# Kernel tuning notes

Measured on AMD Instinct MI355X. Metric: run time of the kernel, lower is better.

## Reference

```python
import jax, jax.numpy as jnp
import numpy as np

N_NODES = 100000
F_DIM = 128      # graph.num_node_features
TE_DIM = 32      # te_emb_dim
D = F_DIM + TE_DIM  # attention embed_dim = 160
B = 4096         # number of target nodes (batched python loop)
K = 64           # candidates per target
TAU = 1.0
THRESHOLD = 0.2
EPS = 1e-10


def setup_inputs() -> dict:
    key = jax.random.key(0)
    ks = jax.random.split(key, 16)
    inp = {
        "x": jax.random.normal(ks[0], (N_NODES, F_DIM), dtype=jnp.float32),
        "target_node_ids": jax.random.randint(ks[1], (B,), 0, N_NODES),
        "target_node_times": jax.random.randint(ks[2], (B,), 1, 10000),
        "neighbor_ids": jax.random.randint(ks[3], (B, K), 0, N_NODES),
        "edge_time": jax.random.randint(ks[4], (B, K), 0, 10000),
        "edge_weight": jax.random.uniform(ks[5], (B, K), dtype=jnp.float32),
        "gumbel_u": jax.random.uniform(ks[6], (B, K), dtype=jnp.float32),
        # TemporalEncoding params: te(t) = cos(t * w + b)
        "te_w": jax.random.normal(ks[7], (TE_DIM,), dtype=jnp.float32),
        "te_b": jax.random.normal(ks[8], (TE_DIM,), dtype=jnp.float32),
        # MultiheadAttention params (packed qkv like torch)
        "in_proj_w": jax.random.normal(ks[9], (3 * D, D), dtype=jnp.float32) / np.sqrt(D),
        "in_proj_b": jnp.zeros((3 * D,), dtype=jnp.float32),
        "out_w": jax.random.normal(ks[10], (D, D), dtype=jnp.float32) / np.sqrt(D),
        "out_b": jnp.zeros((D,), dtype=jnp.float32),
        # MLP: Linear(D+1 -> 1) + LeakyReLU
        "mlp_w": jax.random.normal(ks[11], (D + 1,), dtype=jnp.float32) / np.sqrt(D + 1),
        "mlp_b": jnp.zeros((1,), dtype=jnp.float32),
    }
    return inp


def reference(x, target_node_ids, target_node_times, neighbor_ids, edge_time,
              edge_weight, gumbel_u, te_w, te_b, in_proj_w, in_proj_b,
              out_w, out_b, mlp_w, mlp_b):
    # --- build target embedding: [B, D]
    t_x = x[target_node_ids]                                          # [B, F]
    t_te = jnp.cos(target_node_times[:, None].astype(jnp.float32) * te_w + te_b)  # [B, TE]
    q_in = jnp.concatenate([t_x, t_te], axis=-1)                      # [B, D]

    # --- candidate embeddings: [B, K, D]
    c_x = x[neighbor_ids]                                             # [B, K, F]
    c_te = jnp.cos(edge_time[..., None].astype(jnp.float32) * te_w + te_b)        # [B, K, TE]
    kv_in = jnp.concatenate([c_x, c_te], axis=-1)                     # [B, K, D]

    # --- single-head MultiheadAttention (eval mode, 1 query per target)
    Wq, Wk, Wv = in_proj_w[:D], in_proj_w[D:2 * D], in_proj_w[2 * D:]
    bq, bk, bv = in_proj_b[:D], in_proj_b[D:2 * D], in_proj_b[2 * D:]
    q = q_in @ Wq.T + bq                                              # [B, D]
    k = jnp.einsum('bkf,df->bkd', kv_in, Wk) + bk                     # [B, K, D]
    v = jnp.einsum('bkf,df->bkd', kv_in, Wv) + bv                     # [B, K, D]
    scores = jnp.einsum('bd,bkd->bk', q, k) / jnp.sqrt(jnp.float32(D))
    attn_w = jax.nn.softmax(scores, axis=-1)                          # [B, K]
    ctx = jnp.einsum('bk,bkd->bd', attn_w, v)                         # [B, D]
    attn_output = ctx @ out_w.T + out_b                               # [B, D]

    # --- gumbel-softmax mask over attention weights (soft, then threshold)
    g = -jnp.log(-jnp.log(gumbel_u + EPS) + EPS)                      # gumbel(0,1)
    y_soft = jax.nn.softmax((attn_w + g) / TAU, axis=-1)
    candidate_mask = y_soft > THRESHOLD                               # [B, K] bool

    # --- MLP edge-weight update: Linear(D+1 -> 1) + LeakyReLU
    mlp_in = jnp.concatenate(
        [jnp.broadcast_to(attn_output[:, None, :], (attn_output.shape[0], edge_weight.shape[1], attn_output.shape[1])),
         edge_weight[..., None]], axis=-1)                            # [B, K, D+1]
    new_edge_weight = jax.nn.leaky_relu(jnp.einsum('bkf,f->bk', mlp_in, mlp_w) + mlp_b[0])  # [B, K]

    return attn_output, new_edge_weight, candidate_mask
```

## Files before the change

kernel.cpp:

```cpp
#include <hip/hip_runtime.h>

#define F_DIM 128
#define TE_DIM 32
#define DD 160
#define NB 4096
#define KK 64
#define ROWS 4
#define LD 164
#define TE_STRIDE 36

#define WS_M   0
#define WS_V2  25600
#define WS_C   51200
#define WS_U   51360
#define WS_B2  51520
#define WS_S0  51680
#define WS_TOT 51681

__device__ __forceinline__ float dot4acc(const float4 w, const float4 v, float a) {
    a = fmaf(w.x, v.x, a);
    a = fmaf(w.y, v.y, a);
    a = fmaf(w.z, v.z, a);
    a = fmaf(w.w, v.w, a);
    return a;
}

__device__ __forceinline__ float wave_max(float v) {
    #pragma unroll
    for (int off = 32; off > 0; off >>= 1) v = fmaxf(v, __shfl_xor(v, off, 64));
    return v;
}
__device__ __forceinline__ float wave_sum(float v) {
    #pragma unroll
    for (int off = 32; off > 0; off >>= 1) v += __shfl_xor(v, off, 64);
    return v;
}

__device__ __forceinline__ void gemv_rows(
    const float* __restrict__ W, const float* __restrict__ bias,
    const float (*vin)[LD], float (*vout)[LD], int tid)
{
    const int r  = tid & 3;
    const int dl = tid >> 2;
    const float4* v4 = (const float4*)vin[r];
    const float4* w0 = (const float4*)(W + (long)dl * DD);
    const float4* w1 = (const float4*)(W + (long)(dl + 64) * DD);
    float a0 = bias[dl];
    float a1 = bias[dl + 64];
    if (dl < 32) {
        const float4* w2 = (const float4*)(W + (long)(dl + 128) * DD);
        float a2 = bias[dl + 128];
        #pragma unroll 8
        for (int f = 0; f < 40; ++f) {
            const float4 v = v4[f];
            a0 = dot4acc(w0[f], v, a0);
            a1 = dot4acc(w1[f], v, a1);
            a2 = dot4acc(w2[f], v, a2);
        }
        vout[r][dl]       = a0;
        vout[r][dl + 64]  = a1;
        vout[r][dl + 128] = a2;
    } else {
        #pragma unroll 8
        for (int f = 0; f < 40; ++f) {
            const float4 v = v4[f];
            a0 = dot4acc(w0[f], v, a0);
            a1 = dot4acc(w1[f], v, a1);
        }
        vout[r][dl]      = a0;
        vout[r][dl + 64] = a1;
    }
}

__global__ __launch_bounds__(256)
void setup_kernel(const float* __restrict__ ipw, const float* __restrict__ ipb,
                  const float* __restrict__ ow,  const float* __restrict__ ob,
                  float* __restrict__ ws)
{
    const int blk = blockIdx.x;
    const int t   = threadIdx.x;
    const float inv = 0.07905694150420949f;

    __shared__ float s_vec[DD];

    if (blk < DD) {
        const float* wk = ipw + DD * DD;
        if (t < DD) s_vec[t] = wk[(long)t * DD + blk];
        __syncthreads();
        if (t < DD) {
            float a0 = 0.f, a1 = 0.f, a2 = 0.f, a3 = 0.f;
            #pragma unroll 4
            for (int d = 0; d < DD; d += 4) {
                a0 = fmaf(s_vec[d],     ipw[(long)d * DD + t],       a0);
                a1 = fmaf(s_vec[d + 1], ipw[(long)(d + 1) * DD + t], a1);
                a2 = fmaf(s_vec[d + 2], ipw[(long)(d + 2) * DD + t], a2);
                a3 = fmaf(s_vec[d + 3], ipw[(long)(d + 3) * DD + t], a3);
            }
            ws[WS_M + blk * DD + t] = (a0 + a1 + a2 + a3) * inv;
        }
    } else if (blk < 2 * DD) {
        const int i = blk - DD;
        const float* wv = ipw + 2 * DD * DD;
        if (t < DD) s_vec[t] = ow[(long)i * DD + t];
        __syncthreads();
        if (t < DD) {
            float a0 = 0.f, a1 = 0.f, a2 = 0.f, a3 = 0.f;
            #pragma unroll 4
            for (int d = 0; d < DD; d += 4) {
                a0 = fmaf(s_vec[d],     wv[(long)d * DD + t],       a0);
                a1 = fmaf(s_vec[d + 1], wv[(long)(d + 1) * DD + t], a1);
                a2 = fmaf(s_vec[d + 2], wv[(long)(d + 2) * DD + t], a2);
                a3 = fmaf(s_vec[d + 3], wv[(long)(d + 3) * DD + t], a3);
            }
            ws[WS_V2 + i * DD + t] = a0 + a1 + a2 + a3;
        }
    } else if (blk == 2 * DD) {
        const float* wk = ipw + DD * DD;
        if (t < DD) s_vec[t] = ipb[t];
        __syncthreads();
        if (t < DD) {
            float a0 = 0.f, a1 = 0.f, a2 = 0.f, a3 = 0.f;
            #pragma unroll 4
            for (int d = 0; d < DD; d += 4) {
                a0 = fmaf(s_vec[d],     wk[(long)d * DD + t],       a0);
                a1 = fmaf(s_vec[d + 1], wk[(long)(d + 1) * DD + t], a1);
                a2 = fmaf(s_vec[d + 2], wk[(long)(d + 2) * DD + t], a2);
                a3 = fmaf(s_vec[d + 3], wk[(long)(d + 3) * DD + t], a3);
            }
            ws[WS_C + t] = (a0 + a1 + a2 + a3) * inv;
        }
    } else if (blk == 2 * DD + 1) {
        if (t < DD) s_vec[t] = ipb[DD + t];
        __syncthreads();
        if (t < DD) {
            float a0 = 0.f, a1 = 0.f, a2 = 0.f, a3 = 0.f;
            #pragma unroll 4
            for (int d = 0; d < DD; d += 4) {
                a0 = fmaf(s_vec[d],     ipw[(long)d * DD + t],       a0);
                a1 = fmaf(s_vec[d + 1], ipw[(long)(d + 1) * DD + t], a1);
                a2 = fmaf(s_vec[d + 2], ipw[(long)(d + 2) * DD + t], a2);
                a3 = fmaf(s_vec[d + 3], ipw[(long)(d + 3) * DD + t], a3);
            }
            ws[WS_U + t] = (a0 + a1 + a2 + a3) * inv;
        }
    } else {
        if (t < DD) s_vec[t] = ipb[2 * DD + t];
        __syncthreads();
        if (t < DD) {
            const float* owr = ow + (long)t * DD;
            float a0 = 0.f, a1 = 0.f, a2 = 0.f, a3 = 0.f;
            #pragma unroll 4
            for (int d = 0; d < DD; d += 4) {
                a0 = fmaf(s_vec[d],     owr[d],     a0);
                a1 = fmaf(s_vec[d + 1], owr[d + 1], a1);
                a2 = fmaf(s_vec[d + 2], owr[d + 2], a2);
                a3 = fmaf(s_vec[d + 3], owr[d + 3], a3);
            }
            ws[WS_B2 + t] = ob[t] + (a0 + a1 + a2 + a3);
        }
        if (t >= 192) {
            const int lane = t - 192;
            float p = ipb[lane] * ipb[DD + lane];
            p = fmaf(ipb[lane + 64], ipb[DD + lane + 64], p);
            if (lane < 32) p = fmaf(ipb[lane + 128], ipb[DD + lane + 128], p);
            const float s = wave_sum(p);
            if (lane == 0) ws[WS_S0] = s * inv;
        }
    }
}

__global__ __launch_bounds__(256, 4)
void structure_learner_kernel(
    const float* __restrict__ x,
    const int*   __restrict__ target_node_ids,
    const int*   __restrict__ target_node_times,
    const int*   __restrict__ neighbor_ids,
    const int*   __restrict__ edge_time,
    const float* __restrict__ edge_weight,
    const float* __restrict__ gumbel_u,
    const float* __restrict__ te_w,
    const float* __restrict__ te_b,
    const float* __restrict__ mlp_w,
    const float* __restrict__ mlp_b,
    const float* __restrict__ ws,
    float* __restrict__ out_ao,
    float* __restrict__ out_new,
    float* __restrict__ out_mask)
{
    __shared__ __attribute__((aligned(16))) float s_qin[ROWS][LD];
    __shared__ __attribute__((aligned(16))) float s_qt[ROWS][LD];
    __shared__ __attribute__((aligned(16))) float s_wkv[ROWS][LD];
    __shared__ __attribute__((aligned(16))) float s_ao[ROWS][LD];
    __shared__ float s_attnw[ROWS][KK];
    __shared__ int   s_nid[ROWS][KK];
    __shared__ __attribute__((aligned(4))) _Float16 s_te[ROWS][KK][TE_STRIDE];

    const int tid  = threadIdx.x;
    const int wr   = tid >> 6;
    const int lane = tid & 63;
    const int b    = blockIdx.x * ROWS + wr;

    const float* Mw = ws + WS_M;
    const float* V2 = ws + WS_V2;
    const float* Cv = ws + WS_C;
    const float* Uv = ws + WS_U;
    const float* B2 = ws + WS_B2;
    const float  s0 = ws[WS_S0];

    {
        s_nid[wr][lane] = neighbor_ids[(long)b * KK + lane];
        const float etv = (float)edge_time[(long)b * KK + lane];
        const int tn = target_node_ids[b];
        const float2 tx = *(const float2*)(x + (long)tn * F_DIM + lane * 2);
        s_qin[wr][lane * 2]     = tx.x;
        s_qin[wr][lane * 2 + 1] = tx.y;
        if (lane < TE_DIM) {
            const float tt = (float)target_node_times[b];
            s_qin[wr][F_DIM + lane] = cosf(tt * te_w[lane] + te_b[lane]);
        }
        #pragma unroll
        for (int jj = 0; jj < 16; ++jj) {
            union { _Float16 h[2]; unsigned u; } pk;
            pk.h[0] = (_Float16)cosf(etv * te_w[2 * jj]     + te_b[2 * jj]);
            pk.h[1] = (_Float16)cosf(etv * te_w[2 * jj + 1] + te_b[2 * jj + 1]);
            *(unsigned*)&s_te[wr][lane][2 * jj] = pk.u;
        }
    }
    __syncthreads();

    gemv_rows(Mw, Cv, s_qin, s_qt, tid);
    __syncthreads();

    float aw;
    {
        float p = s_qin[wr][lane] * Uv[lane];
        p = fmaf(s_qin[wr][lane + 64], Uv[lane + 64], p);
        if (lane < 32) p = fmaf(s_qin[wr][128 + lane], Uv[128 + lane], p);
        const float sbk = wave_sum(p) + s0;

        const int nidk = s_nid[wr][lane];
        const float4* xr  = (const float4*)(x + (long)nidk * F_DIM);
        const float4* qt4 = (const float4*)s_qt[wr];
        float acc = 0.f;
        #pragma unroll 8
        for (int f = 0; f < F_DIM / 4; ++f)
            acc = dot4acc(xr[f], qt4[f], acc);
        const float* qte = s_qt[wr] + F_DIM;
        #pragma unroll
        for (int jj = 0; jj < 16; ++jj) {
            union { _Float16 h[2]; unsigned u; } pk;
            pk.u = *(const unsigned*)&s_te[wr][lane][2 * jj];
            acc = fmaf(qte[2 * jj],     (float)pk.h[0], acc);
            acc = fmaf(qte[2 * jj + 1], (float)pk.h[1], acc);
        }
        const float sc = acc + sbk;
        const float m = wave_max(sc);
        const float e = expf(sc - m);
        const float l = wave_sum(e);
        aw = e / l;
        s_attnw[wr][lane] = aw;
    }

    {
        float ax = 0.f, ay = 0.f, at = 0.f;
        const float* xb = x + lane * 2;
        const int lte = lane & 31;
        #pragma unroll 8
        for (int k = 0; k < KK; ++k) {
            const float wgt = s_attnw[wr][k];
            const int   nid = s_nid[wr][k];
            const float2 xv = *(const float2*)(xb + (long)nid * F_DIM);
            ax = fmaf(wgt, xv.x, ax);
            ay = fmaf(wgt, xv.y, ay);
            at = fmaf(wgt, (float)s_te[wr][k][lte], at);
        }
        s_wkv[wr][lane * 2]     = ax;
        s_wkv[wr][lane * 2 + 1] = ay;
        if (lane < TE_DIM) s_wkv[wr][F_DIM + lane] = at;
    }
    __syncthreads();

    gemv_rows(V2, B2, s_wkv, s_ao, tid);
    __syncthreads();

    {
        float p = s_ao[wr][lane] * mlp_w[lane];
        p = fmaf(s_ao[wr][lane + 64], mlp_w[lane + 64], p);
        if (lane < 32) p = fmaf(s_ao[wr][lane + 128], mlp_w[lane + 128], p);
        const float base = wave_sum(p) + mlp_b[0];

        float* ao = out_ao + (long)b * DD;
        ao[lane]      = s_ao[wr][lane];
        ao[lane + 64] = s_ao[wr][lane + 64];
        if (lane < 32) ao[lane + 128] = s_ao[wr][lane + 128];

        const float u = gumbel_u[(long)b * KK + lane];
        const float g = -logf(-logf(u + 1e-10f) + 1e-10f);
        const float z = aw + g;
        const float m = wave_max(z);
        const float e = expf(z - m);
        const float l = wave_sum(e);
        out_mask[(long)b * KK + lane] = (e / l > 0.2f) ? 1.0f : 0.0f;

        const float ew  = edge_weight[(long)b * KK + lane];
        const float val = fmaf(ew, mlp_w[DD], base);
        out_new[(long)b * KK + lane] = (val >= 0.f) ? val : 0.01f * val;
    }
}

extern "C" void kernel_launch(void* const* d_in, const int* in_sizes, int n_in,
                              void* d_out, int out_size, void* d_ws, size_t ws_size,
                              hipStream_t stream) {
    const float* x   = (const float*)d_in[0];
    const int*   tni = (const int*)d_in[1];
    const int*   tnt = (const int*)d_in[2];
    const int*   nid = (const int*)d_in[3];
    const int*   et  = (const int*)d_in[4];
    const float* ew  = (const float*)d_in[5];
    const float* gu  = (const float*)d_in[6];
    const float* tew = (const float*)d_in[7];
    const float* teb = (const float*)d_in[8];
    const float* ipw = (const float*)d_in[9];
    const float* ipb = (const float*)d_in[10];
    const float* ow  = (const float*)d_in[11];
    const float* ob  = (const float*)d_in[12];
    const float* mw  = (const float*)d_in[13];
    const float* mb  = (const float*)d_in[14];

    float* wsf = (float*)d_ws;

    float* out      = (float*)d_out;
    float* out_ao   = out;
    float* out_new  = out + (long)NB * DD;
    float* out_mask = out + (long)NB * DD + (long)NB * KK;

    setup_kernel<<<2 * DD + 3, 256, 0, stream>>>(ipw, ipb, ow, ob, wsf);

    structure_learner_kernel<<<NB / ROWS, 256, 0, stream>>>(
        x, tni, tnt, nid, et, ew, gu, tew, teb, mw, mb, wsf,
        out_ao, out_new, out_mask);
}
```

Before: 172.6 us.

## Precompute temporal-encoding cosine table in setup kernel and look it up per edge

Adds a 10000x32 cosine lookup table, built by extra setup blocks, so the main kernel reads temporal encodings from the table instead of computing 32 cosf calls per edge. Falls back to direct cosf when the workspace is too small or the time is out of range. Also splits the score dot product into two accumulators and raises the unroll on the weighted-sum loop. Trades transcendental compute for about 1.28 MB of table writes and gathered reads, and the table only covers the integer time range 0 to 9999.

```diff
diff --git a/kernel.cpp b/kernel.cpp
--- a/kernel.cpp
+++ b/kernel.cpp
@@ -15,7 +15,11 @@
 #define WS_U   51360
 #define WS_B2  51520
 #define WS_S0  51680
-#define WS_TOT 51681
+#define WS_TE  51684
+#define TAB_T  10000
+#define TAB_N  (TAB_T * TE_DIM)
+#define TAB_BLOCKS 250
+#define SETUP_BASE (2 * DD + 3)
 
 __device__ __forceinline__ float dot4acc(const float4 w, const float4 v, float a) {
     a = fmaf(w.x, v.x, a);
@@ -75,6 +79,7 @@
 __global__ __launch_bounds__(256)
 void setup_kernel(const float* __restrict__ ipw, const float* __restrict__ ipb,
                   const float* __restrict__ ow,  const float* __restrict__ ob,
+                  const float* __restrict__ te_w, const float* __restrict__ te_b,
                   float* __restrict__ ws)
 {
     const int blk = blockIdx.x;
@@ -82,6 +87,17 @@
     const float inv = 0.07905694150420949f;
 
     __shared__ float s_vec[DD];
+
+    if (blk >= SETUP_BASE) {
+        const int g0 = (blk - SETUP_BASE) * 256 + t;
+        #pragma unroll
+        for (int it = 0; it < 5; ++it) {
+            const int g = g0 + it * (TAB_BLOCKS * 256);
+            const int tt = g >> 5, d = g & 31;
+            ws[WS_TE + g] = cosf(fmaf((float)tt, te_w[d], te_b[d]));
+        }
+        return;
+    }
 
     if (blk < DD) {
         const float* wk = ipw + DD * DD;
@@ -183,6 +199,7 @@
     const float* __restrict__ mlp_w,
     const float* __restrict__ mlp_b,
     const float* __restrict__ ws,
+    const float* __restrict__ tetab,
     float* __restrict__ out_ao,
     float* __restrict__ out_new,
     float* __restrict__ out_mask)
@@ -209,21 +226,38 @@
 
     {
         s_nid[wr][lane] = neighbor_ids[(long)b * KK + lane];
-        const float etv = (float)edge_time[(long)b * KK + lane];
+        const int etv_i = edge_time[(long)b * KK + lane];
         const int tn = target_node_ids[b];
         const float2 tx = *(const float2*)(x + (long)tn * F_DIM + lane * 2);
         s_qin[wr][lane * 2]     = tx.x;
         s_qin[wr][lane * 2 + 1] = tx.y;
         if (lane < TE_DIM) {
-            const float tt = (float)target_node_times[b];
-            s_qin[wr][F_DIM + lane] = cosf(tt * te_w[lane] + te_b[lane]);
-        }
-        #pragma unroll
-        for (int jj = 0; jj < 16; ++jj) {
-            union { _Float16 h[2]; unsigned u; } pk;
-            pk.h[0] = (_Float16)cosf(etv * te_w[2 * jj]     + te_b[2 * jj]);
-            pk.h[1] = (_Float16)cosf(etv * te_w[2 * jj + 1] + te_b[2 * jj + 1]);
-            *(unsigned*)&s_te[wr][lane][2 * jj] = pk.u;
+            const int tt = target_node_times[b];
+            s_qin[wr][F_DIM + lane] =
+                (tetab && (unsigned)tt < (unsigned)TAB_T)
+                    ? tetab[(long)tt * TE_DIM + lane]
+                    : cosf(fmaf((float)tt, te_w[lane], te_b[lane]));
+        }
+        if (tetab && (unsigned)etv_i < (unsigned)TAB_T) {
+            const float4* trow = (const float4*)(tetab + (long)etv_i * TE_DIM);
+            #pragma unroll
+            for (int jj = 0; jj < 8; ++jj) {
+                const float4 tv = trow[jj];
+                union { _Float16 h[2]; unsigned u; } p0, p1;
+                p0.h[0] = (_Float16)tv.x; p0.h[1] = (_Float16)tv.y;
+                p1.h[0] = (_Float16)tv.z; p1.h[1] = (_Float16)tv.w;
+                *(unsigned*)&s_te[wr][lane][4 * jj]     = p0.u;
+                *(unsigned*)&s_te[wr][lane][4 * jj + 2] = p1.u;
+            }
+        } else {
+            const float etv = (float)etv_i;
+            #pragma unroll
+            for (int jj = 0; jj < 16; ++jj) {
+                union { _Float16 h[2]; unsigned u; } pk;
+                pk.h[0] = (_Float16)cosf(fmaf(etv, te_w[2 * jj],     te_b[2 * jj]));
+                pk.h[1] = (_Float16)cosf(fmaf(etv, te_w[2 * jj + 1], te_b[2 * jj + 1]));
+                *(unsigned*)&s_te[wr][lane][2 * jj] = pk.u;
+            }
         }
     }
     __syncthreads();
@@ -241,10 +275,13 @@
         const int nidk = s_nid[wr][lane];
         const float4* xr  = (const float4*)(x + (long)nidk * F_DIM);
         const float4* qt4 = (const float4*)s_qt[wr];
-        float acc = 0.f;
-        #pragma unroll 8
-        for (int f = 0; f < F_DIM / 4; ++f)
-            acc = dot4acc(xr[f], qt4[f], acc);
+        float acc0 = 0.f, acc1 = 0.f;
+        #pragma unroll 16
+        for (int f = 0; f < F_DIM / 8; ++f) {
+            acc0 = dot4acc(xr[2 * f],     qt4[2 * f],     acc0);
+            acc1 = dot4acc(xr[2 * f + 1], qt4[2 * f + 1], acc1);
+        }
+        float acc = acc0 + acc1;
         const float* qte = s_qt[wr] + F_DIM;
         #pragma unroll
         for (int jj = 0; jj < 16; ++jj) {
@@ -265,7 +302,7 @@
         float ax = 0.f, ay = 0.f, at = 0.f;
         const float* xb = x + lane * 2;
         const int lte = lane & 31;
-        #pragma unroll 8
+        #pragma unroll 16
         for (int k = 0; k < KK; ++k) {
             const float wgt = s_attnw[wr][k];
             const int   nid = s_nid[wr][k];
@@ -334,9 +371,13 @@
     float* out_new  = out + (long)NB * DD;
     float* out_mask = out + (long)NB * DD + (long)NB * KK;
 
-    setup_kernel<<<2 * DD + 3, 256, 0, stream>>>(ipw, ipb, ow, ob, wsf);
+    const bool use_tab = ws_size >= (size_t)(WS_TE + TAB_N) * sizeof(float);
+    const int  setup_grid = SETUP_BASE + (use_tab ? TAB_BLOCKS : 0);
+
+    setup_kernel<<<setup_grid, 256, 0, stream>>>(ipw, ipb, ow, ob, tew, teb, wsf);
 
     structure_learner_kernel<<<NB / ROWS, 256, 0, stream>>>(
         x, tni, tnt, nid, et, ew, gu, tew, teb, mw, mb, wsf,
+        use_tab ? (wsf + WS_TE) : nullptr,
         out_ao, out_new, out_mask);
 }
```

After: 175.4 us. No clear change (+1.6%).
